# Kernel tuning notes

Measured on AMD Instinct MI355X. Metric: run time of the kernel, lower is better.

## Reference

```python
import jax, jax.numpy as jnp
import numpy as np
import math

HEADS = 16
D_MODEL = 1024
D_K = D_MODEL // HEADS


def setup_inputs() -> dict:
    key = jax.random.key(0)
    ks = jax.random.split(key, 11)
    B, S = 2, 2048
    s = 1.0 / math.sqrt(D_MODEL)
    return {
        "q": jax.random.normal(ks[0], (B, S, D_MODEL), jnp.float32),
        "k": jax.random.normal(ks[1], (B, S, D_MODEL), jnp.float32),
        "v": jax.random.normal(ks[2], (B, S, D_MODEL), jnp.float32),
        "Wq": jax.random.normal(ks[3], (D_MODEL, D_MODEL), jnp.float32) * s,
        "bq": jax.random.normal(ks[4], (D_MODEL,), jnp.float32) * s,
        "Wk": jax.random.normal(ks[5], (D_MODEL, D_MODEL), jnp.float32) * s,
        "bk": jax.random.normal(ks[6], (D_MODEL,), jnp.float32) * s,
        "Wv": jax.random.normal(ks[7], (D_MODEL, D_MODEL), jnp.float32) * s,
        "bv": jax.random.normal(ks[8], (D_MODEL,), jnp.float32) * s,
        "Wo": jax.random.normal(ks[9], (D_MODEL, D_MODEL), jnp.float32) * s,
        "bo": jax.random.normal(ks[10], (D_MODEL,), jnp.float32) * s,
    }


def reference(q, k, v, Wq, bq, Wk, bk, Wv, bv, Wo, bo):
    B, S, _ = q.shape
    # linear projections, split heads: [B, H, S, d_k]
    def proj(x, W, b):
        y = x @ W.T + b
        return y.reshape(B, -1, HEADS, D_K).transpose(0, 2, 1, 3)
    qh, kh, vh = proj(q, Wq, bq), proj(k, Wk, bk), proj(v, Wv, bv)
    # abs-modified scaled dot-product attention (no mask, eval -> no dropout)
    scores = jnp.abs(jnp.einsum("bhsd,bhtd->bhst", qh, kh) / math.sqrt(D_K))
    attn = jax.nn.softmax(scores, axis=-1)
    out = jnp.einsum("bhst,bhtd->bhsd", attn, vh)
    concat = out.transpose(0, 2, 1, 3).reshape(B, S, D_MODEL)
    return concat @ Wo.T + bo
```

## Files before the change

### kernel.cpp

```cpp
#include <hip/hip_runtime.h>

#define HEADS 16
#define DK 64
#define DM 1024
#define SEQ 2048
#define BATCH 2

using bf16x8 = __attribute__((ext_vector_type(8))) short;
using short4v = __attribute__((ext_vector_type(4))) short;
using f32x4 = __attribute__((ext_vector_type(4))) float;

static __device__ __forceinline__ short f2bf(float x) {
  union { float f; unsigned u; } c;
  c.f = x;
  unsigned r = (c.u + 0x7FFFu + ((c.u >> 16) & 1u)) >> 16;
  return (short)r;
}

static __device__ __forceinline__ void gload_lds16(const void* g, void* l) {
  __builtin_amdgcn_global_load_lds(
      (const __attribute__((address_space(1))) void*)g,
      (__attribute__((address_space(3))) void*)l, 16, 0, 0);
}

__global__ __launch_bounds__(256) void cvt7(
    const float* __restrict__ s0, const float* __restrict__ s1,
    const float* __restrict__ s2, const float* __restrict__ s3,
    const float* __restrict__ s4, const float* __restrict__ s5,
    const float* __restrict__ s6, short* d0, short* d1, short* d2, short* d3,
    short* d4, short* d5, short* d6) {
  const int y = blockIdx.y;
  const float* s;
  short* d;
  int n;
  switch (y) {
    case 0: s = s0; d = d0; n = BATCH * SEQ * DM; break;
    case 1: s = s1; d = d1; n = BATCH * SEQ * DM; break;
    case 2: s = s2; d = d2; n = BATCH * SEQ * DM; break;
    case 3: s = s3; d = d3; n = DM * DM; break;
    case 4: s = s4; d = d4; n = DM * DM; break;
    case 5: s = s5; d = d5; n = DM * DM; break;
    default: s = s6; d = d6; n = DM * DM; break;
  }
  const int n4 = n >> 2;
  const int stride = gridDim.x * 256;
  for (int i = blockIdx.x * 256 + threadIdx.x; i < n4; i += stride) {
    float4 v = ((const float4*)s)[i];
    short4v o;
    o.x = f2bf(v.x);
    o.y = f2bf(v.y);
    o.z = f2bf(v.z);
    o.w = f2bf(v.w);
    ((short4v*)d)[i] = o;
  }
}

__global__ __launch_bounds__(256) void proj_qkv(
    const short* __restrict__ Aq, const short* __restrict__ Ak,
    const short* __restrict__ Av, const short* __restrict__ Wq_,
    const short* __restrict__ Wk_, const short* __restrict__ Wv_,
    const float* __restrict__ bq, const float* __restrict__ bk,
    const float* __restrict__ bv, short* __restrict__ Qh,
    short* __restrict__ Kh, short* __restrict__ Vt) {
  __shared__ short smem[128 * 136];
  short* As = smem;
  short* Ws = smem + 8192;

  const int z = blockIdx.z;
  const short* A = z == 0 ? Aq : z == 1 ? Ak : Av;
  const short* W = z == 0 ? Wq_ : z == 1 ? Wk_ : Wv_;
  const float* bias = z == 0 ? bq : z == 1 ? bk : bv;
  short* C = z == 0 ? Qh : z == 1 ? Kh : Vt;
  const bool tr = (z == 2);

  const int tid = threadIdx.x;
  const int wave = tid >> 6, lane = tid & 63;
  const int quad = lane >> 4, l15 = lane & 15;
  const int n0 = blockIdx.x * 128, m0 = blockIdx.y * 128;
  const int mh = (wave & 1) * 64, nh = (wave >> 1) * 64;
  const int ldr = lane >> 3, ldc = lane & 7;

  f32x4 acc[4][4] = {};

  for (int k0 = 0; k0 < 1024; k0 += 64) {
    __syncthreads();
#pragma unroll
    for (int i = 0; i < 8; ++i) {
      int seg = wave * 8 + i;
      int r = (seg & 15) * 8 + ldr;
      int kb = ldc ^ (r & 7);
      if (seg < 16)
        gload_lds16(&A[(size_t)(m0 + r) * 1024 + k0 + kb * 8], &As[seg * 512]);
      else
        gload_lds16(&W[(size_t)(n0 + r) * 1024 + k0 + kb * 8],
                    &Ws[(seg - 16) * 512]);
    }
    __syncthreads();
#pragma unroll
    for (int ks = 0; ks < 2; ++ks) {
      bf16x8 a[4], b[4];
      int kb = ks * 4 + quad;
#pragma unroll
      for (int f = 0; f < 4; ++f) {
        int rm = mh + f * 16 + l15;
        int rn = nh + f * 16 + l15;
        a[f] = *(const bf16x8*)&As[rm * 64 + (kb ^ (rm & 7)) * 8];
        b[f] = *(const bf16x8*)&Ws[rn * 64 + (kb ^ (rn & 7)) * 8];
      }
#pragma unroll
      for (int mf = 0; mf < 4; ++mf)
#pragma unroll
        for (int nf = 0; nf < 4; ++nf)
          acc[mf][nf] = __builtin_amdgcn_mfma_f32_16x16x32_bf16(
              a[mf], b[nf], acc[mf][nf], 0, 0, 0);
    }
  }

  float bvv[4];
#pragma unroll
  for (int nf = 0; nf < 4; ++nf) bvv[nf] = bias[n0 + nh + nf * 16 + l15];

  __syncthreads();
  short* Cb = smem;

  if (!tr) {
#pragma unroll
    for (int mf = 0; mf < 4; ++mf)
#pragma unroll
      for (int nf = 0; nf < 4; ++nf)
#pragma unroll
        for (int r = 0; r < 4; ++r)
          Cb[(mh + mf * 16 + quad * 4 + r) * 136 + nh + nf * 16 + l15] =
              f2bf(acc[mf][nf][r] + bvv[nf]);
    __syncthreads();
#pragma unroll
    for (int j = 0; j < 8; ++j) {
      int cid = tid + 256 * j;
      int row = cid >> 4, cb = cid & 15;
      bf16x8 v = *(const bf16x8*)&Cb[row * 136 + cb * 8];
      int m = m0 + row, n = n0 + cb * 8;
      int b = m >> 11, s = m & (SEQ - 1), h = n >> 6, d = n & 63;
      *(bf16x8*)&C[((size_t)(b * HEADS + h) * SEQ + s) * DK + d] = v;
    }
  } else {
#pragma unroll
    for (int mf = 0; mf < 4; ++mf)
#pragma unroll
      for (int nf = 0; nf < 4; ++nf) {
        short4v p;
        p.x = f2bf(acc[mf][nf][0] + bvv[nf]);
        p.y = f2bf(acc[mf][nf][1] + bvv[nf]);
        p.z = f2bf(acc[mf][nf][2] + bvv[nf]);
        p.w = f2bf(acc[mf][nf][3] + bvv[nf]);
        *(short4v*)&Cb[(nh + nf * 16 + l15) * 136 + mh + mf * 16 + quad * 4] =
            p;
      }
    __syncthreads();
#pragma unroll
    for (int j = 0; j < 8; ++j) {
      int cid = tid + 256 * j;
      int row = cid >> 4, cb = cid & 15;
      bf16x8 v = *(const bf16x8*)&Cb[row * 136 + cb * 8];
      int n = n0 + row, m = m0 + cb * 8;
      int b = m >> 11, s = m & (SEQ - 1), h = n >> 6, d = n & 63;
      *(bf16x8*)&C[((size_t)(b * HEADS + h) * DK + d) * SEQ + s] = v;
    }
  }
}

__global__ __launch_bounds__(256) void proj_out(const short* __restrict__ A,
                                                const short* __restrict__ W,
                                                const float* __restrict__ bias,
                                                float* __restrict__ C) {
  __shared__ short smem[128 * 136];
  short* As = smem;
  short* Ws = smem + 8192;

  const int tid = threadIdx.x;
  const int wave = tid >> 6, lane = tid & 63;
  const int quad = lane >> 4, l15 = lane & 15;
  const int n0 = blockIdx.x * 128, m0 = blockIdx.y * 128;
  const int mh = (wave & 1) * 64, nh = (wave >> 1) * 64;
  const int ldr = lane >> 3, ldc = lane & 7;

  f32x4 acc[4][4] = {};

  for (int k0 = 0; k0 < 1024; k0 += 64) {
    __syncthreads();
#pragma unroll
    for (int i = 0; i < 8; ++i) {
      int seg = wave * 8 + i;
      int r = (seg & 15) * 8 + ldr;
      int kb = ldc ^ (r & 7);
      if (seg < 16)
        gload_lds16(&A[(size_t)(m0 + r) * 1024 + k0 + kb * 8], &As[seg * 512]);
      else
        gload_lds16(&W[(size_t)(n0 + r) * 1024 + k0 + kb * 8],
                    &Ws[(seg - 16) * 512]);
    }
    __syncthreads();
#pragma unroll
    for (int ks = 0; ks < 2; ++ks) {
      bf16x8 a[4], b[4];
      int kb = ks * 4 + quad;
#pragma unroll
      for (int f = 0; f < 4; ++f) {
        int rm = mh + f * 16 + l15;
        int rn = nh + f * 16 + l15;
        a[f] = *(const bf16x8*)&As[rm * 64 + (kb ^ (rm & 7)) * 8];
        b[f] = *(const bf16x8*)&Ws[rn * 64 + (kb ^ (rn & 7)) * 8];
      }
#pragma unroll
      for (int mf = 0; mf < 4; ++mf)
#pragma unroll
        for (int nf = 0; nf < 4; ++nf)
          acc[mf][nf] = __builtin_amdgcn_mfma_f32_16x16x32_bf16(
              a[mf], b[nf], acc[mf][nf], 0, 0, 0);
    }
  }

  float bvv[4];
#pragma unroll
  for (int nf = 0; nf < 4; ++nf) bvv[nf] = bias[n0 + nh + nf * 16 + l15];
#pragma unroll
  for (int mf = 0; mf < 4; ++mf)
#pragma unroll
    for (int nf = 0; nf < 4; ++nf)
#pragma unroll
      for (int r = 0; r < 4; ++r)
        C[(size_t)(m0 + mh + mf * 16 + quad * 4 + r) * 1024 + n0 + nh +
          nf * 16 + l15] = acc[mf][nf][r] + bvv[nf];
}

__global__ __launch_bounds__(256) void attn_mfma(const short* __restrict__ Qh,
                                                 const short* __restrict__ Kh,
                                                 const short* __restrict__ VtG,
                                                 short* __restrict__ concat) {
  __shared__ short Ks[64 * 64];
  __shared__ short Vt[64 * 64];
  __shared__ short Ps[128 * 64];

  const int tid = threadIdx.x;
  const int wave = tid >> 6, lane = tid & 63;
  const int quad = lane >> 4, l15 = lane & 15;
  const int bh = blockIdx.y;
  const int q0 = blockIdx.x * 128;
  const size_t base = (size_t)bh * SEQ * DK;
  const int ldr = lane >> 3, ldc = lane & 7;

  bf16x8 qf[2][2];
#pragma unroll
  for (int mf = 0; mf < 2; ++mf)
#pragma unroll
    for (int ks = 0; ks < 2; ++ks)
      qf[mf][ks] =
          *(const bf16x8*)&Qh[base +
                              (size_t)(q0 + wave * 32 + mf * 16 + l15) * 64 +
                              ks * 32 + quad * 8];

  f32x4 O[2][4] = {};
  float lsum[2][4] = {};

  for (int kt = 0; kt < SEQ / 64; ++kt) {
    __syncthreads();
#pragma unroll
    for (int i = 0; i < 2; ++i) {
      int seg = wave * 2 + i;
      int row = seg * 8 + ldr;
      int kb = ldc ^ (row & 7);
      gload_lds16(&Kh[base + (size_t)(kt * 64 + row) * 64 + kb * 8],
                  &Ks[seg * 512]);
      gload_lds16(&VtG[base + (size_t)row * SEQ + kt * 64 + kb * 8],
                  &Vt[seg * 512]);
    }
    __syncthreads();

    f32x4 sf[2][4] = {};
#pragma unroll
    for (int ks = 0; ks < 2; ++ks) {
      bf16x8 bfr[4];
      int kb = ks * 4 + quad;
#pragma unroll
      for (int nf = 0; nf < 4; ++nf) {
        int n = nf * 16 + l15;
        bfr[nf] = *(const bf16x8*)&Ks[n * 64 + (kb ^ (n & 7)) * 8];
      }
#pragma unroll
      for (int mf = 0; mf < 2; ++mf)
#pragma unroll
        for (int nf = 0; nf < 4; ++nf)
          sf[mf][nf] = __builtin_amdgcn_mfma_f32_16x16x32_bf16(
              qf[mf][ks], bfr[nf], sf[mf][nf], 0, 0, 0);
    }

    const int h2 = l15 >> 3, lo3 = l15 & 7;
#pragma unroll
    for (int mf = 0; mf < 2; ++mf)
#pragma unroll
      for (int nf = 0; nf < 4; ++nf) {
        const int ch = 2 * nf + h2;
#pragma unroll
        for (int r = 0; r < 4; ++r) {
          float e = __expf(fabsf(sf[mf][nf][r]) * 0.125f);
          lsum[mf][r] += e;
          int row = wave * 32 + mf * 16 + quad * 4 + r;
          Ps[(row << 6) + ((ch ^ ((row >> 1) & 7)) << 3) + lo3] = f2bf(e);
        }
      }
    __threadfence_block();

#pragma unroll
    for (int ks = 0; ks < 2; ++ks) {
      bf16x8 av[2], bvv[4];
      int kb = ks * 4 + quad;
#pragma unroll
      for (int mf = 0; mf < 2; ++mf) {
        int row = wave * 32 + mf * 16 + l15;
        av[mf] = *(const bf16x8*)&Ps[(row << 6) +
                                     ((kb ^ ((row >> 1) & 7)) << 3)];
      }
#pragma unroll
      for (int nf = 0; nf < 4; ++nf) {
        int n = nf * 16 + l15;
        bvv[nf] = *(const bf16x8*)&Vt[n * 64 + (kb ^ (n & 7)) * 8];
      }
#pragma unroll
      for (int mf = 0; mf < 2; ++mf)
#pragma unroll
        for (int nf = 0; nf < 4; ++nf)
          O[mf][nf] = __builtin_amdgcn_mfma_f32_16x16x32_bf16(
              av[mf], bvv[nf], O[mf][nf], 0, 0, 0);
    }
  }

  float inv[2][4];
#pragma unroll
  for (int mf = 0; mf < 2; ++mf)
#pragma unroll
    for (int r = 0; r < 4; ++r) {
      float s = lsum[mf][r];
#pragma unroll
      for (int x = 1; x < 16; x <<= 1) s += __shfl_xor(s, x, 64);
      inv[mf][r] = 1.f / s;
    }

  __syncthreads();
  const int h2 = l15 >> 3, lo3 = l15 & 7;
#pragma unroll
  for (int mf = 0; mf < 2; ++mf)
#pragma unroll
    for (int nf = 0; nf < 4; ++nf) {
      const int ch = 2 * nf + h2;
#pragma unroll
      for (int r = 0; r < 4; ++r) {
        int row = wave * 32 + mf * 16 + quad * 4 + r;
        Ps[(row << 6) + ((ch ^ ((row >> 1) & 7)) << 3) + lo3] =
            f2bf(O[mf][nf][r] * inv[mf][r]);
      }
    }
  __syncthreads();
  const int b = bh >> 4, h = bh & 15;
#pragma unroll
  for (int j = 0; j < 4; ++j) {
    int cid = tid + 256 * j;
    int row = cid >> 3, cb = cid & 7;
    bf16x8 v = *(const bf16x8*)&Ps[(row << 6) + ((cb ^ ((row >> 1) & 7)) << 3)];
    *(bf16x8*)&concat[((size_t)(b * SEQ + q0 + row)) * DM + h * 64 + cb * 8] =
        v;
  }
}

extern "C" void kernel_launch(void* const* d_in, const int* in_sizes, int n_in,
                              void* d_out, int out_size, void* d_ws,
                              size_t ws_size, hipStream_t stream) {
  const float* q = (const float*)d_in[0];
  const float* k = (const float*)d_in[1];
  const float* v = (const float*)d_in[2];
  const float* Wq = (const float*)d_in[3];
  const float* bq = (const float*)d_in[4];
  const float* Wk = (const float*)d_in[5];
  const float* bk = (const float*)d_in[6];
  const float* Wv = (const float*)d_in[7];
  const float* bv = (const float*)d_in[8];
  const float* Wo = (const float*)d_in[9];
  const float* bo = (const float*)d_in[10];

  short* ws = (short*)d_ws;
  const size_t T4 = (size_t)BATCH * SEQ * DM;
  const size_t T1 = (size_t)DM * DM;
  short* qb = ws;
  short* kb_ = ws + T4;
  short* vb = ws + 2 * T4;
  short* Wqb = ws + 3 * T4;
  short* Wkb = Wqb + T1;
  short* Wvb = Wqb + 2 * T1;
  short* Wob = Wqb + 3 * T1;
  short* Qh = Wqb + 4 * T1;
  short* Kh = Qh + T4;
  short* VtG = Qh + 2 * T4;
  short* cc = Qh + 3 * T4;

  cvt7<<<dim3(1024, 7), 256, 0, stream>>>(q, k, v, Wq, Wk, Wv, Wo, qb, kb_, vb,
                                          Wqb, Wkb, Wvb, Wob);

  proj_qkv<<<dim3(DM / 128, (BATCH * SEQ) / 128, 3), 256, 0, stream>>>(
      qb, kb_, vb, Wqb, Wkb, Wvb, bq, bk, bv, Qh, Kh, VtG);

  attn_mfma<<<dim3(SEQ / 128, BATCH * HEADS), 256, 0, stream>>>(Qh, Kh, VtG,
                                                                cc);

  proj_out<<<dim3(DM / 128, (BATCH * SEQ) / 128), 256, 0, stream>>>(
      cc, Wob, bo, (float*)d_out);
}
```

Baseline: 243.5 us.

## Double-buffer attention K/V tiles, shrink tiles, pack bf16 conversions

Attention now uses 64-query, 128-thread blocks and double-buffers K and V tiles in LDS, so the next tile's global-to-LDS load is issued while the current one is computed. This hides load latency and doubles the grid. The exp is rewritten as exp2 with a folded constant, and P is written with packed 32-bit bf16 stores. The output projection uses 128x64 tiles to raise block count, and the converters use a packed bf16 conversion helper. The key rows are permuted when staging, and the PV step must still match, which is a correctness risk.

```diff
diff --git a/kernel.cpp b/kernel.cpp
--- a/kernel.cpp
+++ b/kernel.cpp
@@ -15,6 +15,23 @@
   c.f = x;
   unsigned r = (c.u + 0x7FFFu + ((c.u >> 16) & 1u)) >> 16;
   return (short)r;
+}
+
+static __device__ __forceinline__ unsigned pk2bf(float lo, float hi) {
+#if __has_builtin(__builtin_amdgcn_cvt_pk_bf16_f32)
+  auto t = __builtin_amdgcn_cvt_pk_bf16_f32(lo, hi);
+  if constexpr (sizeof(t) == 4) {
+    unsigned u;
+    __builtin_memcpy(&u, &t, 4);
+    return u;
+  } else {
+    return (unsigned)(unsigned short)f2bf(lo) |
+           ((unsigned)(unsigned short)f2bf(hi) << 16);
+  }
+#else
+  return (unsigned)(unsigned short)f2bf(lo) |
+         ((unsigned)(unsigned short)f2bf(hi) << 16);
+#endif
 }
 
 static __device__ __forceinline__ void gload_lds16(const void* g, void* l) {
@@ -46,12 +63,10 @@
   const int stride = gridDim.x * 256;
   for (int i = blockIdx.x * 256 + threadIdx.x; i < n4; i += stride) {
     float4 v = ((const float4*)s)[i];
-    short4v o;
-    o.x = f2bf(v.x);
-    o.y = f2bf(v.y);
-    o.z = f2bf(v.z);
-    o.w = f2bf(v.w);
-    ((short4v*)d)[i] = o;
+    uint2 o;
+    o.x = pk2bf(v.x, v.y);
+    o.y = pk2bf(v.z, v.w);
+    ((uint2*)d)[i] = o;
   }
 }
 
@@ -127,11 +142,17 @@
 #pragma unroll
     for (int mf = 0; mf < 4; ++mf)
 #pragma unroll
-      for (int nf = 0; nf < 4; ++nf)
-#pragma unroll
-        for (int r = 0; r < 4; ++r)
-          Cb[(mh + mf * 16 + quad * 4 + r) * 136 + nh + nf * 16 + l15] =
-              f2bf(acc[mf][nf][r] + bvv[nf]);
+      for (int r = 0; r < 4; ++r) {
+        int row = mh + mf * 16 + quad * 4 + r;
+        unsigned u01 =
+            pk2bf(acc[mf][0][r] + bvv[0], acc[mf][1][r] + bvv[1]);
+        unsigned u23 =
+            pk2bf(acc[mf][2][r] + bvv[2], acc[mf][3][r] + bvv[3]);
+        Cb[row * 136 + nh + l15] = (short)u01;
+        Cb[row * 136 + nh + 16 + l15] = (short)(u01 >> 16);
+        Cb[row * 136 + nh + 32 + l15] = (short)u23;
+        Cb[row * 136 + nh + 48 + l15] = (short)(u23 >> 16);
+      }
     __syncthreads();
 #pragma unroll
     for (int j = 0; j < 8; ++j) {
@@ -147,13 +168,13 @@
     for (int mf = 0; mf < 4; ++mf)
 #pragma unroll
       for (int nf = 0; nf < 4; ++nf) {
-        short4v p;
-        p.x = f2bf(acc[mf][nf][0] + bvv[nf]);
-        p.y = f2bf(acc[mf][nf][1] + bvv[nf]);
-        p.z = f2bf(acc[mf][nf][2] + bvv[nf]);
-        p.w = f2bf(acc[mf][nf][3] + bvv[nf]);
-        *(short4v*)&Cb[(nh + nf * 16 + l15) * 136 + mh + mf * 16 + quad * 4] =
-            p;
+        unsigned u01 =
+            pk2bf(acc[mf][nf][0] + bvv[nf], acc[mf][nf][1] + bvv[nf]);
+        unsigned u23 =
+            pk2bf(acc[mf][nf][2] + bvv[nf], acc[mf][nf][3] + bvv[nf]);
+        int base_ = (nh + nf * 16 + l15) * 136 + mh + mf * 16 + quad * 4;
+        *(unsigned*)&Cb[base_] = u01;
+        *(unsigned*)&Cb[base_ + 2] = u23;
       }
     __syncthreads();
 #pragma unroll
@@ -172,79 +193,85 @@
                                                 const short* __restrict__ W,
                                                 const float* __restrict__ bias,
                                                 float* __restrict__ C) {
-  __shared__ short smem[128 * 136];
+  __shared__ short smem[12288];
   short* As = smem;
   short* Ws = smem + 8192;
 
   const int tid = threadIdx.x;
   const int wave = tid >> 6, lane = tid & 63;
   const int quad = lane >> 4, l15 = lane & 15;
-  const int n0 = blockIdx.x * 128, m0 = blockIdx.y * 128;
-  const int mh = (wave & 1) * 64, nh = (wave >> 1) * 64;
+  const int n0 = blockIdx.x * 64, m0 = blockIdx.y * 128;
+  const int mh = (wave & 1) * 64, nh = (wave >> 1) * 32;
   const int ldr = lane >> 3, ldc = lane & 7;
 
-  f32x4 acc[4][4] = {};
+  f32x4 acc[4][2] = {};
 
   for (int k0 = 0; k0 < 1024; k0 += 64) {
     __syncthreads();
 #pragma unroll
-    for (int i = 0; i < 8; ++i) {
-      int seg = wave * 8 + i;
-      int r = (seg & 15) * 8 + ldr;
-      int kb = ldc ^ (r & 7);
-      if (seg < 16)
+    for (int i = 0; i < 6; ++i) {
+      int seg = wave * 6 + i;
+      if (seg < 16) {
+        int r = seg * 8 + ldr;
+        int kb = ldc ^ (r & 7);
         gload_lds16(&A[(size_t)(m0 + r) * 1024 + k0 + kb * 8], &As[seg * 512]);
-      else
+      } else {
+        int r = (seg - 16) * 8 + ldr;
+        int kb = ldc ^ (r & 7);
         gload_lds16(&W[(size_t)(n0 + r) * 1024 + k0 + kb * 8],
                     &Ws[(seg - 16) * 512]);
+      }
     }
     __syncthreads();
 #pragma unroll
     for (int ks = 0; ks < 2; ++ks) {
-      bf16x8 a[4], b[4];
+      bf16x8 a[4], b[2];
       int kb = ks * 4 + quad;
 #pragma unroll
       for (int f = 0; f < 4; ++f) {
         int rm = mh + f * 16 + l15;
+        a[f] = *(const bf16x8*)&As[rm * 64 + (kb ^ (rm & 7)) * 8];
+      }
+#pragma unroll
+      for (int f = 0; f < 2; ++f) {
         int rn = nh + f * 16 + l15;
-        a[f] = *(const bf16x8*)&As[rm * 64 + (kb ^ (rm & 7)) * 8];
         b[f] = *(const bf16x8*)&Ws[rn * 64 + (kb ^ (rn & 7)) * 8];
       }
 #pragma unroll
       for (int mf = 0; mf < 4; ++mf)
 #pragma unroll
-        for (int nf = 0; nf < 4; ++nf)
+        for (int nf = 0; nf < 2; ++nf)
           acc[mf][nf] = __builtin_amdgcn_mfma_f32_16x16x32_bf16(
               a[mf], b[nf], acc[mf][nf], 0, 0, 0);
     }
   }
 
-  float bvv[4];
-#pragma unroll
-  for (int nf = 0; nf < 4; ++nf) bvv[nf] = bias[n0 + nh + nf * 16 + l15];
+  float bvv[2];
+#pragma unroll
+  for (int nf = 0; nf < 2; ++nf) bvv[nf] = bias[n0 + nh + nf * 16 + l15];
 #pragma unroll
   for (int mf = 0; mf < 4; ++mf)
 #pragma unroll
-    for (int nf = 0; nf < 4; ++nf)
+    for (int nf = 0; nf < 2; ++nf)
 #pragma unroll
       for (int r = 0; r < 4; ++r)
         C[(size_t)(m0 + mh + mf * 16 + quad * 4 + r) * 1024 + n0 + nh +
           nf * 16 + l15] = acc[mf][nf][r] + bvv[nf];
 }
 
-__global__ __launch_bounds__(256) void attn_mfma(const short* __restrict__ Qh,
+__global__ __launch_bounds__(128) void attn_mfma(const short* __restrict__ Qh,
                                                  const short* __restrict__ Kh,
                                                  const short* __restrict__ VtG,
                                                  short* __restrict__ concat) {
-  __shared__ short Ks[64 * 64];
-  __shared__ short Vt[64 * 64];
-  __shared__ short Ps[128 * 64];
+  __shared__ short Ks[2][64 * 64];
+  __shared__ short Vt[2][64 * 64];
+  __shared__ short Ps[64 * 64];
 
   const int tid = threadIdx.x;
   const int wave = tid >> 6, lane = tid & 63;
   const int quad = lane >> 4, l15 = lane & 15;
   const int bh = blockIdx.y;
-  const int q0 = blockIdx.x * 128;
+  const int q0 = blockIdx.x * 64;
   const size_t base = (size_t)bh * SEQ * DK;
   const int ldr = lane >> 3, ldc = lane & 7;
 
@@ -261,19 +288,28 @@
   f32x4 O[2][4] = {};
   float lsum[2][4] = {};
 
+#define STAGE_TILE(kt_, buf_)                                              \
+  {                                                                        \
+    _Pragma("unroll") for (int i_ = 0; i_ < 4; ++i_) {                     \
+      int seg = wave * 4 + i_;                                             \
+      int row = seg * 8 + ldr;                                             \
+      int kb = ldc ^ (row & 7);                                            \
+      int key = 2 * (row & 15) + ((row >> 4) & 1) + 32 * (row >> 5);       \
+      gload_lds16(&Kh[base + (size_t)((kt_)*64 + key) * 64 + kb * 8],      \
+                  &Ks[buf_][seg * 512]);                                   \
+      gload_lds16(&VtG[base + (size_t)row * SEQ + (kt_)*64 + kb * 8],      \
+                  &Vt[buf_][seg * 512]);                                   \
+    }                                                                      \
+  }
+
+  STAGE_TILE(0, 0);
+
+  const float CE = 0.18033688011112042f;
+
   for (int kt = 0; kt < SEQ / 64; ++kt) {
-    __syncthreads();
-#pragma unroll
-    for (int i = 0; i < 2; ++i) {
-      int seg = wave * 2 + i;
-      int row = seg * 8 + ldr;
-      int kb = ldc ^ (row & 7);
-      gload_lds16(&Kh[base + (size_t)(kt * 64 + row) * 64 + kb * 8],
-                  &Ks[seg * 512]);
-      gload_lds16(&VtG[base + (size_t)row * SEQ + kt * 64 + kb * 8],
-                  &Vt[seg * 512]);
-    }
-    __syncthreads();
+    const int cur = kt & 1;
+    __syncthreads();
+    if (kt + 1 < SEQ / 64) STAGE_TILE(kt + 1, cur ^ 1);
 
     f32x4 sf[2][4] = {};
 #pragma unroll
@@ -283,7 +319,7 @@
 #pragma unroll
       for (int nf = 0; nf < 4; ++nf) {
         int n = nf * 16 + l15;
-        bfr[nf] = *(const bf16x8*)&Ks[n * 64 + (kb ^ (n & 7)) * 8];
+        bfr[nf] = *(const bf16x8*)&Ks[cur][n * 64 + (kb ^ (n & 7)) * 8];
       }
 #pragma unroll
       for (int mf = 0; mf < 2; ++mf)
@@ -293,19 +329,23 @@
               qf[mf][ks], bfr[nf], sf[mf][nf], 0, 0, 0);
     }
 
-    const int h2 = l15 >> 3, lo3 = l15 & 7;
 #pragma unroll
     for (int mf = 0; mf < 2; ++mf)
 #pragma unroll
-      for (int nf = 0; nf < 4; ++nf) {
-        const int ch = 2 * nf + h2;
-#pragma unroll
-        for (int r = 0; r < 4; ++r) {
-          float e = __expf(fabsf(sf[mf][nf][r]) * 0.125f);
-          lsum[mf][r] += e;
-          int row = wave * 32 + mf * 16 + quad * 4 + r;
-          Ps[(row << 6) + ((ch ^ ((row >> 1) & 7)) << 3) + lo3] = f2bf(e);
-        }
+      for (int r = 0; r < 4; ++r) {
+        float e0 = exp2f(fabsf(sf[mf][0][r]) * CE);
+        float e1 = exp2f(fabsf(sf[mf][1][r]) * CE);
+        float e2 = exp2f(fabsf(sf[mf][2][r]) * CE);
+        float e3 = exp2f(fabsf(sf[mf][3][r]) * CE);
+        lsum[mf][r] += (e0 + e1) + (e2 + e3);
+        unsigned u01 = pk2bf(e0, e1);
+        unsigned u23 = pk2bf(e2, e3);
+        int row = wave * 32 + mf * 16 + quad * 4 + r;
+        int sw = (row >> 1) & 7;
+        int off = (2 * l15) & 7;
+        short* rp = &Ps[row * 64];
+        *(unsigned*)&rp[(((l15 >> 2) ^ sw) << 3) + off] = u01;
+        *(unsigned*)&rp[(((4 + (l15 >> 2)) ^ sw) << 3) + off] = u23;
       }
     __threadfence_block();
 
@@ -316,13 +356,13 @@
 #pragma unroll
       for (int mf = 0; mf < 2; ++mf) {
         int row = wave * 32 + mf * 16 + l15;
-        av[mf] = *(const bf16x8*)&Ps[(row << 6) +
-                                     ((kb ^ ((row >> 1) & 7)) << 3)];
+        av[mf] =
+            *(const bf16x8*)&Ps[row * 64 + ((kb ^ ((row >> 1) & 7)) << 3)];
       }
 #pragma unroll
       for (int nf = 0; nf < 4; ++nf) {
         int n = nf * 16 + l15;
-        bvv[nf] = *(const bf16x8*)&Vt[n * 64 + (kb ^ (n & 7)) * 8];
+        bvv[nf] = *(const bf16x8*)&Vt[cur][n * 64 + (kb ^ (n & 7)) * 8];
       }
 #pragma unroll
       for (int mf = 0; mf < 2; ++mf)
@@ -345,29 +385,33 @@
     }
 
   __syncthreads();
-  const int h2 = l15 >> 3, lo3 = l15 & 7;
 #pragma unroll
   for (int mf = 0; mf < 2; ++mf)
 #pragma unroll
-    for (int nf = 0; nf < 4; ++nf) {
-      const int ch = 2 * nf + h2;
-#pragma unroll
-      for (int r = 0; r < 4; ++r) {
-        int row = wave * 32 + mf * 16 + quad * 4 + r;
-        Ps[(row << 6) + ((ch ^ ((row >> 1) & 7)) << 3) + lo3] =
-            f2bf(O[mf][nf][r] * inv[mf][r]);
-      }
+    for (int r = 0; r < 4; ++r) {
+      unsigned u01 =
+          pk2bf(O[mf][0][r] * inv[mf][r], O[mf][1][r] * inv[mf][r]);
+      unsigned u23 =
+          pk2bf(O[mf][2][r] * inv[mf][r], O[mf][3][r] * inv[mf][r]);
+      int row = wave * 32 + mf * 16 + quad * 4 + r;
+      int sw = (row >> 1) & 7;
+      short* rp = &Ps[row * 64];
+      rp[((((l15) >> 3) ^ sw) << 3) + (l15 & 7)] = (short)u01;
+      rp[((((16 + l15) >> 3) ^ sw) << 3) + (l15 & 7)] = (short)(u01 >> 16);
+      rp[((((32 + l15) >> 3) ^ sw) << 3) + (l15 & 7)] = (short)u23;
+      rp[((((48 + l15) >> 3) ^ sw) << 3) + (l15 & 7)] = (short)(u23 >> 16);
     }
   __syncthreads();
   const int b = bh >> 4, h = bh & 15;
 #pragma unroll
   for (int j = 0; j < 4; ++j) {
-    int cid = tid + 256 * j;
+    int cid = tid + 128 * j;
     int row = cid >> 3, cb = cid & 7;
-    bf16x8 v = *(const bf16x8*)&Ps[(row << 6) + ((cb ^ ((row >> 1) & 7)) << 3)];
+    bf16x8 v = *(const bf16x8*)&Ps[row * 64 + ((cb ^ ((row >> 1) & 7)) << 3)];
     *(bf16x8*)&concat[((size_t)(b * SEQ + q0 + row)) * DM + h * 64 + cb * 8] =
         v;
   }
+#undef STAGE_TILE
 }
 
 extern "C" void kernel_launch(void* const* d_in, const int* in_sizes, int n_in,
@@ -406,9 +450,9 @@
   proj_qkv<<<dim3(DM / 128, (BATCH * SEQ) / 128, 3), 256, 0, stream>>>(
       qb, kb_, vb, Wqb, Wkb, Wvb, bq, bk, bv, Qh, Kh, VtG);
 
-  attn_mfma<<<dim3(SEQ / 128, BATCH * HEADS), 256, 0, stream>>>(Qh, Kh, VtG,
-                                                                cc);
-
-  proj_out<<<dim3(DM / 128, (BATCH * SEQ) / 128), 256, 0, stream>>>(
+  attn_mfma<<<dim3(SEQ / 64, BATCH * HEADS), 128, 0, stream>>>(Qh, Kh, VtG,
+                                                               cc);
+
+  proj_out<<<dim3(DM / 64, (BATCH * SEQ) / 128), 256, 0, stream>>>(
       cc, Wob, bo, (float*)d_out);
 }
```

Measured after the change: 266.7 us. +9.5%, slower.
